# Kernel tuning notes

Hardware: AMD Instinct MI355X
Metric: run time of the kernel (lower is better)

The kernel has to match this reference:

```python
import jax, jax.numpy as jnp
import numpy as np

VOC, TOPIC, EMB, BATCH = 128000, 512, 1024, 1024

def setup_inputs() -> dict:
    key = jax.random.key(0)
    k1, k2, k3 = jax.random.split(key, 3)
    x = jax.random.normal(k1, (TOPIC, BATCH), dtype=jnp.float32)
    beta0 = jax.random.normal(k2, (VOC, EMB), dtype=jnp.float32)
    beta_t = jax.random.normal(k3, (TOPIC, EMB), dtype=jnp.float32) * 0.02  # nn.init.normal_(std=0.02)
    return {"x": x, "beta0": beta0, "beta_t": beta_t, "t": 0}

def reference(x, beta0, beta_t, t):
    # w: [voc, topic] = beta0 [voc, emb] @ beta_t.T [emb, topic]
    # (the t==0 branch and else branch are identical in the source)
    w = jnp.einsum('ve,te->vt', beta0, beta_t)
    w = jax.nn.softmax(w, axis=0)  # softmax over vocab dim (dim=0)
    # out: [voc, batch]
    return jnp.einsum('vt,tb->vb', w, x)
```

## Files before the change

kernel.cpp:

```cpp
#include <hip/hip_runtime.h>

typedef _Float16 f16x8 __attribute__((ext_vector_type(8)));
typedef float    f32x4 __attribute__((ext_vector_type(4)));
typedef unsigned short u16;

#define VOC   128000
#define TOPIC 512
#define EMB   1024
#define BATCH 1024
#define ROWB  128

__device__ __forceinline__ int swz(int row, int kbyte) {
    return row * ROWB + (kbyte ^ ((row & 7) << 4));
}
__device__ __forceinline__ int xcd_swz(int bid, int nwg) {
    return (bid & 7) * (nwg >> 3) + (bid >> 3);
}
union H2U { _Float16 h; u16 u; };

__global__ void cvt_betat_kernel(const float* __restrict__ betat, u16* __restrict__ bt16) {
    const size_t g = (size_t)blockIdx.x * 256 + threadIdx.x;
    const float4* src = reinterpret_cast<const float4*>(betat) + g * 2;
    float4 a = src[0], b = src[1];
    f16x8 h;
    h[0]=(_Float16)a.x; h[1]=(_Float16)a.y; h[2]=(_Float16)a.z; h[3]=(_Float16)a.w;
    h[4]=(_Float16)b.x; h[5]=(_Float16)b.y; h[6]=(_Float16)b.z; h[7]=(_Float16)b.w;
    *(reinterpret_cast<f16x8*>(bt16) + g) = h;
}

__global__ __launch_bounds__(512, 2) void gemm1_kernel(
    const float* __restrict__ beta0, const u16* __restrict__ bt16,
    u16* __restrict__ Eg, size_t TSTR, int RSTR, float* __restrict__ sg)
{
    __shared__ char lds[49152];
    char* ldsA = lds;
    char* ldsB = lds + 16384;

    const int tid  = threadIdx.x;
    const int lane = tid & 63;
    const int wid  = tid >> 6;
    const int wr = wid >> 2, wc = wid & 3;
    const int lr = lane & 15, lk = lane >> 4;
    const int srow8  = lane >> 3;
    const int schunk = ((lane & 7) ^ srow8) * 8;

    const int bid  = xcd_swz(blockIdx.x, gridDim.x);
    const int t0   = (bid & 1) * 256;
    const int tile = bid >> 1;
    const int v0   = tile * 128;

    const int arow = tid >> 2;
    const int asp  = (tid & 3) * 2;

    f32x4 acc[4][4] = {};
    float4 rA[4];

    auto loadA = [&](int kt) {
        const float4* g = reinterpret_cast<const float4*>(
            beta0 + (size_t)(v0 + arow) * EMB + kt * 64 + asp * 8);
        rA[0] = g[0]; rA[1] = g[1]; rA[2] = g[2]; rA[3] = g[3];
    };

    loadA(0);

    for (int kt = 0; kt < EMB / 64; ++kt) {
        __syncthreads();
        const u16* bsrc = bt16 + (size_t)(t0 + wid * 8 + srow8) * EMB + kt * 64 + schunk;
        #pragma unroll
        for (int p = 0; p < 4; ++p) {
            __builtin_amdgcn_global_load_lds(
                (const __attribute__((address_space(1))) unsigned int*)(bsrc + (size_t)p * 64 * EMB),
                (__attribute__((address_space(3))) unsigned int*)(ldsB + (p * 64 + wid * 8) * ROWB),
                16, 0, 0);
        }
        {
            f16x8 h;
            h[0]=(_Float16)rA[0].x; h[1]=(_Float16)rA[0].y; h[2]=(_Float16)rA[0].z; h[3]=(_Float16)rA[0].w;
            h[4]=(_Float16)rA[1].x; h[5]=(_Float16)rA[1].y; h[6]=(_Float16)rA[1].z; h[7]=(_Float16)rA[1].w;
            *reinterpret_cast<f16x8*>(ldsA + swz(arow, asp * 16)) = h;
            f16x8 h2;
            h2[0]=(_Float16)rA[2].x; h2[1]=(_Float16)rA[2].y; h2[2]=(_Float16)rA[2].z; h2[3]=(_Float16)rA[2].w;
            h2[4]=(_Float16)rA[3].x; h2[5]=(_Float16)rA[3].y; h2[6]=(_Float16)rA[3].z; h2[7]=(_Float16)rA[3].w;
            *reinterpret_cast<f16x8*>(ldsA + swz(arow, (asp + 1) * 16)) = h2;
        }
        if (kt + 1 < EMB / 64) loadA(kt + 1);
        __syncthreads();
        #pragma unroll
        for (int ks = 0; ks < 2; ++ks) {
            f16x8 af[4], bf[4];
            #pragma unroll
            for (int m = 0; m < 4; ++m)
                af[m] = *reinterpret_cast<const f16x8*>(ldsA + swz(wr * 64 + m * 16 + lr, ks * 64 + lk * 16));
            #pragma unroll
            for (int n = 0; n < 4; ++n)
                bf[n] = *reinterpret_cast<const f16x8*>(ldsB + swz(wc * 64 + n * 16 + lr, ks * 64 + lk * 16));
            #pragma unroll
            for (int m = 0; m < 4; ++m)
                #pragma unroll
                for (int n = 0; n < 4; ++n)
                    acc[m][n] = __builtin_amdgcn_mfma_f32_16x16x32_f16(
                        af[m], bf[n], acc[m][n], 0, 0, 0);
        }
    }

    __syncthreads();
    u16* ldsE = reinterpret_cast<u16*>(lds);
    float csum = 0.f;
    #pragma unroll
    for (int c = 0; c < 2; ++c) {
        if (wr == c) {
            #pragma unroll
            for (int m = 0; m < 4; ++m)
              #pragma unroll
              for (int n = 0; n < 4; ++n)
                #pragma unroll
                for (int r = 0; r < 4; ++r) {
                    const int row = m * 16 + lk * 4 + r;
                    const int col = wc * 64 + n * 16 + lr;
                    H2U cv; cv.h = (_Float16)__expf(acc[m][n][r]);
                    ldsE[row * 264 + col] = cv.u;
                }
        }
        __syncthreads();
        {
            const int row8 = tid >> 3, seg = tid & 7;
            const int4* srcp = reinterpret_cast<const int4*>(&ldsE[row8 * 264 + seg * 32]);
            u16* dst = Eg + tile * TSTR + (size_t)(c * 64 + row8) * RSTR + t0 + seg * 32;
            int4 v0v = srcp[0], v1v = srcp[1], v2v = srcp[2], v3v = srcp[3];
            int4* dp = reinterpret_cast<int4*>(dst);
            dp[0] = v0v; dp[1] = v1v; dp[2] = v2v; dp[3] = v3v;
        }
        if (tid < 256) {
            float s = 0.f;
            for (int r = 0; r < 64; ++r) { H2U cv; cv.u = ldsE[r * 264 + tid]; s += (float)cv.h; }
            csum += s;
        }
        __syncthreads();
    }
    if (tid < 256) atomicAdd(sg + t0 + tid, csum);
}

__global__ void xst_kernel(const float* __restrict__ x, const float* __restrict__ s,
                           u16* __restrict__ xsT)
{
    __shared__ float tile[32][33];
    const int b0 = blockIdx.x * 32, t0 = blockIdx.y * 32;
    const int tx = threadIdx.x, ty = threadIdx.y;
    tile[ty][tx] = x[(size_t)(t0 + ty) * BATCH + b0 + tx];
    __syncthreads();
    const float sc = 65536.0f / s[t0 + tx];
    H2U cv; cv.h = (_Float16)(tile[tx][ty] * sc);
    xsT[(size_t)(b0 + ty) * TOPIC + t0 + tx] = cv.u;
}

__global__ __launch_bounds__(512, 2) void gemm2a_kernel(
    const u16* __restrict__ Eg, size_t TSTR, int RSTR,
    const u16* __restrict__ xsT, float* __restrict__ out, int c0, int nch)
{
    __shared__ char lds[49152];
    char* ldsA = lds;
    char* ldsB = lds + 16384;

    const int tid  = threadIdx.x;
    const int lane = tid & 63;
    const int wid  = tid >> 6;
    const int wr = wid >> 2, wc = wid & 3;
    const int lr = lane & 15, lk = lane >> 4;
    const int srow8  = lane >> 3;
    const int schunk = ((lane & 7) ^ srow8) * 8;

    const int bid   = xcd_swz(blockIdx.x, gridDim.x);
    const int tile  = bid / nch;
    const int chunk = bid % nch;
    const int b0    = c0 + chunk * 256;
    const int v0    = tile * 128;
    const u16* Et   = Eg + tile * TSTR;

    f32x4 acc[4][4] = {};

    for (int kt = 0; kt < TOPIC / 64; ++kt) {
        const int k0 = kt * 64;
        __syncthreads();
        #pragma unroll
        for (int p = 0; p < 2; ++p) {
            const int rbase = p * 64 + wid * 8;
            __builtin_amdgcn_global_load_lds(
                (const __attribute__((address_space(1))) unsigned int*)
                    (Et + (size_t)(rbase + srow8) * RSTR + k0 + schunk),
                (__attribute__((address_space(3))) unsigned int*)(ldsA + rbase * ROWB),
                16, 0, 0);
        }
        #pragma unroll
        for (int p = 0; p < 4; ++p) {
            const int rbase = p * 64 + wid * 8;
            __builtin_amdgcn_global_load_lds(
                (const __attribute__((address_space(1))) unsigned int*)
                    (xsT + (size_t)(b0 + rbase + srow8) * TOPIC + k0 + schunk),
                (__attribute__((address_space(3))) unsigned int*)(ldsB + rbase * ROWB),
                16, 0, 0);
        }
        __syncthreads();
        #pragma unroll
        for (int ks = 0; ks < 2; ++ks) {
            f16x8 af[4], bf[4];
            #pragma unroll
            for (int m = 0; m < 4; ++m)
                af[m] = *reinterpret_cast<const f16x8*>(ldsA + swz(wr * 64 + m * 16 + lr, ks * 64 + lk * 16));
            #pragma unroll
            for (int n = 0; n < 4; ++n)
                bf[n] = *reinterpret_cast<const f16x8*>(ldsB + swz(wc * 64 + n * 16 + lr, ks * 64 + lk * 16));
            #pragma unroll
            for (int m = 0; m < 4; ++m)
                #pragma unroll
                for (int n = 0; n < 4; ++n)
                    acc[m][n] = __builtin_amdgcn_mfma_f32_16x16x32_f16(
                        af[m], bf[n], acc[m][n], 0, 0, 0);
        }
    }

    #pragma unroll
    for (int m = 0; m < 4; ++m)
      #pragma unroll
      for (int n = 0; n < 4; ++n)
        #pragma unroll
        for (int r = 0; r < 4; ++r) {
            const int row = wr * 64 + m * 16 + lk * 4 + r;
            const int col = wc * 64 + n * 16 + lr;
            out[(size_t)(v0 + row) * BATCH + b0 + col] = acc[m][n][r] * 0x1p-16f;
        }
}

__global__ __launch_bounds__(512, 1) void gemm2b_kernel(
    const u16* __restrict__ EgBase,
    const u16* __restrict__ xsT, float* __restrict__ out)
{
    __shared__ char ldsB[32768];

    const int tid  = threadIdx.x;
    const int lane = tid & 63;
    const int wid  = tid >> 6;
    const int wr = wid >> 2, wc = wid & 3;
    const int lr = lane & 15, lk = lane >> 4;

    const int bid  = xcd_swz(blockIdx.x, gridDim.x);
    const int tile = bid >> 1;
    const int h    = bid & 1;
    const u16* Et  = EgBase + (size_t)tile * 262144;

    f16x8 af[2][16];
    #pragma unroll
    for (int m = 0; m < 2; ++m) {
        const int row = h * 64 + wr * 32 + m * 16 + lr;
        #pragma unroll
        for (int kb = 0; kb < 16; ++kb)
            af[m][kb] = *reinterpret_cast<const f16x8*>(
                Et + (size_t)row * 2048 + kb * 32 + lk * 8);
    }
    asm volatile("s_waitcnt vmcnt(0)" ::: "memory");
    __syncthreads();

    f32x4 acc[2][4] = {};
    for (int kt = 0; kt < 8; ++kt) {
        __syncthreads();
        {
            const int srow = tid >> 1;
            const int sp   = (tid & 1) * 4;
            const u16* g = xsT + (size_t)srow * TOPIC + kt * 64 + sp * 8;
            const int4* gv = reinterpret_cast<const int4*>(g);
            int4 a = gv[0], b = gv[1], cc = gv[2], d = gv[3];
            *reinterpret_cast<int4*>(ldsB + swz(srow, (sp + 0) * 16)) = a;
            *reinterpret_cast<int4*>(ldsB + swz(srow, (sp + 1) * 16)) = b;
            *reinterpret_cast<int4*>(ldsB + swz(srow, (sp + 2) * 16)) = cc;
            *reinterpret_cast<int4*>(ldsB + swz(srow, (sp + 3) * 16)) = d;
        }
        __syncthreads();
        #pragma unroll
        for (int kk = 0; kk < 2; ++kk) {
            f16x8 bf[4];
            #pragma unroll
            for (int n = 0; n < 4; ++n)
                bf[n] = *reinterpret_cast<const f16x8*>(ldsB + swz(wc * 64 + n * 16 + lr, kk * 64 + lk * 16));
            #pragma unroll
            for (int m = 0; m < 2; ++m)
                #pragma unroll
                for (int n = 0; n < 4; ++n)
                    acc[m][n] = __builtin_amdgcn_mfma_f32_16x16x32_f16(
                        af[m][kt * 2 + kk], bf[n], acc[m][n], 0, 0, 0);
        }
    }

    #pragma unroll
    for (int m = 0; m < 2; ++m)
      #pragma unroll
      for (int n = 0; n < 4; ++n)
        #pragma unroll
        for (int r = 0; r < 4; ++r) {
            const int row = h * 64 + wr * 32 + m * 16 + lk * 4 + r;
            const int col = wc * 64 + n * 16 + lr;
            out[((size_t)tile * 128 + row) * BATCH + col] = acc[m][n][r] * 0x1p-16f;
        }
}

extern "C" void kernel_launch(void* const* d_in, const int* in_sizes, int n_in,
                              void* d_out, int out_size, void* d_ws, size_t ws_size,
                              hipStream_t stream)
{
    const float* x     = (const float*)d_in[0];
    const float* beta0 = (const float*)d_in[1];
    const float* betat = (const float*)d_in[2];
    float* out = (float*)d_out;

    const size_t need_min = 4096 + (size_t)BATCH * TOPIC * 2;
    if (ws_size < need_min) return;
    float* s_g  = (float*)d_ws;
    u16*   buf1 = (u16*)((char*)d_ws + 4096);

    const size_t E_OFF = 4u * 1024u * 1024u;
    const bool big = ws_size >= E_OFF + (size_t)VOC * TOPIC * 2;

    hipMemsetAsync(d_ws, 0, 2048, stream);
    cvt_betat_kernel<<<256, 256, 0, stream>>>(betat, buf1);

    if (big) {
        u16* EgW = (u16*)((char*)d_ws + E_OFF);
        gemm1_kernel<<<2000, 512, 0, stream>>>(beta0, buf1, EgW, (size_t)128 * 512, 512, s_g);
        xst_kernel<<<dim3(BATCH / 32, TOPIC / 32), dim3(32, 32), 0, stream>>>(x, s_g, buf1);
        gemm2a_kernel<<<4000, 512, 0, stream>>>(EgW, (size_t)128 * 512, 512, buf1, out, 0, 4);
    } else {
        u16* EgO = (u16*)d_out;
        gemm1_kernel<<<2000, 512, 0, stream>>>(beta0, buf1, EgO, (size_t)262144, 2048, s_g);
        xst_kernel<<<dim3(BATCH / 32, TOPIC / 32), dim3(32, 32), 0, stream>>>(x, s_g, buf1);
        gemm2a_kernel<<<3000, 512, 0, stream>>>(EgO, (size_t)262144, 2048, buf1, out, 256, 3);
        gemm2b_kernel<<<2000, 512, 0, stream>>>(EgO, buf1, out);
    }
}
```

Baseline: 582.0 us.

## Double-buffer LDS tiles in all three GEMM kernels to overlap loads with MFMA

Adds ping-pong LDS buffers in gemm1, gemm2a and gemm2b so the global-to-LDS loads for the next K tile are issued before the MFMA work on the current tile. The __syncthreads pairs are replaced by raw s_barrier plus explicit vmcnt/lgkmcnt waits. gemm2b also moves to register prefetch of x and raises its launch-bounds occupancy hint to 2. The aim is to hide global load latency. In exchange, LDS per block doubles to 96 KB in gemm1 and gemm2a, which may cut occupancy below the requested 2 blocks per CU. The hand-written waits also risk subtle races.

```diff
diff --git a/kernel.cpp b/kernel.cpp
--- a/kernel.cpp
+++ b/kernel.cpp
@@ -17,6 +17,10 @@
     return (bid & 7) * (nwg >> 3) + (bid >> 3);
 }
 union H2U { _Float16 h; u16 u; };
+
+#define SBAR() asm volatile("s_barrier" ::: "memory")
+#define WVM0() asm volatile("s_waitcnt vmcnt(0)" ::: "memory")
+#define WLG0() asm volatile("s_waitcnt lgkmcnt(0)" ::: "memory")
 
 __global__ void cvt_betat_kernel(const float* __restrict__ betat, u16* __restrict__ bt16) {
     const size_t g = (size_t)blockIdx.x * 256 + threadIdx.x;
@@ -32,9 +36,7 @@
     const float* __restrict__ beta0, const u16* __restrict__ bt16,
     u16* __restrict__ Eg, size_t TSTR, int RSTR, float* __restrict__ sg)
 {
-    __shared__ char lds[49152];
-    char* ldsA = lds;
-    char* ldsB = lds + 16384;
+    __shared__ char lds[98304];
 
     const int tid  = threadIdx.x;
     const int lane = tid & 63;
@@ -60,19 +62,27 @@
             beta0 + (size_t)(v0 + arow) * EMB + kt * 64 + asp * 8);
         rA[0] = g[0]; rA[1] = g[1]; rA[2] = g[2]; rA[3] = g[3];
     };
-
-    loadA(0);
-
-    for (int kt = 0; kt < EMB / 64; ++kt) {
-        __syncthreads();
+    auto issueB = [&](int kt, int buf) {
         const u16* bsrc = bt16 + (size_t)(t0 + wid * 8 + srow8) * EMB + kt * 64 + schunk;
-        #pragma unroll
-        for (int p = 0; p < 4; ++p) {
+        char* dstb = lds + 32768 + buf * 32768;
+        #pragma unroll
+        for (int p = 0; p < 4; ++p)
             __builtin_amdgcn_global_load_lds(
                 (const __attribute__((address_space(1))) unsigned int*)(bsrc + (size_t)p * 64 * EMB),
-                (__attribute__((address_space(3))) unsigned int*)(ldsB + (p * 64 + wid * 8) * ROWB),
+                (__attribute__((address_space(3))) unsigned int*)(dstb + (p * 64 + wid * 8) * ROWB),
                 16, 0, 0);
-        }
+    };
+
+    issueB(0, 0);
+    loadA(0);
+
+    for (int kt = 0; kt < EMB / 64; ++kt) {
+        const int cur = kt & 1;
+        char* ldsA = lds + cur * 16384;
+        char* ldsB = lds + 32768 + cur * 32768;
+
+        SBAR();
+        WVM0();
         {
             f16x8 h;
             h[0]=(_Float16)rA[0].x; h[1]=(_Float16)rA[0].y; h[2]=(_Float16)rA[0].z; h[3]=(_Float16)rA[0].w;
@@ -83,8 +93,9 @@
             h2[4]=(_Float16)rA[3].x; h2[5]=(_Float16)rA[3].y; h2[6]=(_Float16)rA[3].z; h2[7]=(_Float16)rA[3].w;
             *reinterpret_cast<f16x8*>(ldsA + swz(arow, (asp + 1) * 16)) = h2;
         }
-        if (kt + 1 < EMB / 64) loadA(kt + 1);
-        __syncthreads();
+        if (kt + 1 < EMB / 64) { issueB(kt + 1, cur ^ 1); loadA(kt + 1); }
+        WLG0();
+        SBAR();
         #pragma unroll
         for (int ks = 0; ks < 2; ++ks) {
             f16x8 af[4], bf[4];
@@ -157,9 +168,7 @@
     const u16* __restrict__ Eg, size_t TSTR, int RSTR,
     const u16* __restrict__ xsT, float* __restrict__ out, int c0, int nch)
 {
-    __shared__ char lds[49152];
-    char* ldsA = lds;
-    char* ldsB = lds + 16384;
+    __shared__ char lds[98304];
 
     const int tid  = threadIdx.x;
     const int lane = tid & 63;
@@ -178,16 +187,17 @@
 
     f32x4 acc[4][4] = {};
 
-    for (int kt = 0; kt < TOPIC / 64; ++kt) {
+    auto issueAB = [&](int kt, int buf) {
         const int k0 = kt * 64;
-        __syncthreads();
+        char* dA = lds + buf * 16384;
+        char* dB = lds + 32768 + buf * 32768;
         #pragma unroll
         for (int p = 0; p < 2; ++p) {
             const int rbase = p * 64 + wid * 8;
             __builtin_amdgcn_global_load_lds(
                 (const __attribute__((address_space(1))) unsigned int*)
                     (Et + (size_t)(rbase + srow8) * RSTR + k0 + schunk),
-                (__attribute__((address_space(3))) unsigned int*)(ldsA + rbase * ROWB),
+                (__attribute__((address_space(3))) unsigned int*)(dA + rbase * ROWB),
                 16, 0, 0);
         }
         #pragma unroll
@@ -196,10 +206,22 @@
             __builtin_amdgcn_global_load_lds(
                 (const __attribute__((address_space(1))) unsigned int*)
                     (xsT + (size_t)(b0 + rbase + srow8) * TOPIC + k0 + schunk),
-                (__attribute__((address_space(3))) unsigned int*)(ldsB + rbase * ROWB),
+                (__attribute__((address_space(3))) unsigned int*)(dB + rbase * ROWB),
                 16, 0, 0);
         }
-        __syncthreads();
+    };
+
+    issueAB(0, 0);
+
+    for (int kt = 0; kt < TOPIC / 64; ++kt) {
+        const int cur = kt & 1;
+        char* ldsA = lds + cur * 16384;
+        char* ldsB = lds + 32768 + cur * 32768;
+
+        SBAR();
+        WVM0();
+        if (kt + 1 < TOPIC / 64) issueAB(kt + 1, cur ^ 1);
+        SBAR();
         #pragma unroll
         for (int ks = 0; ks < 2; ++ks) {
             f16x8 af[4], bf[4];
@@ -230,11 +252,11 @@
         }
 }
 
-__global__ __launch_bounds__(512, 1) void gemm2b_kernel(
+__global__ __launch_bounds__(512, 2) void gemm2b_kernel(
     const u16* __restrict__ EgBase,
     const u16* __restrict__ xsT, float* __restrict__ out)
 {
-    __shared__ char ldsB[32768];
+    __shared__ char lds[65536];
 
     const int tid  = threadIdx.x;
     const int lane = tid & 63;
@@ -256,24 +278,37 @@
             af[m][kb] = *reinterpret_cast<const f16x8*>(
                 Et + (size_t)row * 2048 + kb * 32 + lk * 8);
     }
-    asm volatile("s_waitcnt vmcnt(0)" ::: "memory");
+    WVM0();
     __syncthreads();
+
+    int4 rX[4];
+    auto loadX = [&](int kt) {
+        const int srow = tid >> 1;
+        const int sp   = (tid & 1) * 4;
+        const int4* gv = reinterpret_cast<const int4*>(
+            xsT + (size_t)srow * TOPIC + kt * 64 + sp * 8);
+        rX[0] = gv[0]; rX[1] = gv[1]; rX[2] = gv[2]; rX[3] = gv[3];
+    };
+    loadX(0);
 
     f32x4 acc[2][4] = {};
     for (int kt = 0; kt < 8; ++kt) {
-        __syncthreads();
+        const int cur = kt & 1;
+        char* ldsB = lds + cur * 32768;
+
+        SBAR();
+        WVM0();
         {
             const int srow = tid >> 1;
             const int sp   = (tid & 1) * 4;
-            const u16* g = xsT + (size_t)srow * TOPIC + kt * 64 + sp * 8;
-            const int4* gv = reinterpret_cast<const int4*>(g);
-            int4 a = gv[0], b = gv[1], cc = gv[2], d = gv[3];
-            *reinterpret_cast<int4*>(ldsB + swz(srow, (sp + 0) * 16)) = a;
-            *reinterpret_cast<int4*>(ldsB + swz(srow, (sp + 1) * 16)) = b;
-            *reinterpret_cast<int4*>(ldsB + swz(srow, (sp + 2) * 16)) = cc;
-            *reinterpret_cast<int4*>(ldsB + swz(srow, (sp + 3) * 16)) = d;
-        }
-        __syncthreads();
+            *reinterpret_cast<int4*>(ldsB + swz(srow, (sp + 0) * 16)) = rX[0];
+            *reinterpret_cast<int4*>(ldsB + swz(srow, (sp + 1) * 16)) = rX[1];
+            *reinterpret_cast<int4*>(ldsB + swz(srow, (sp + 2) * 16)) = rX[2];
+            *reinterpret_cast<int4*>(ldsB + swz(srow, (sp + 3) * 16)) = rX[3];
+        }
+        if (kt + 1 < 8) loadX(kt + 1);
+        WLG0();
+        SBAR();
         #pragma unroll
         for (int kk = 0; kk < 2; ++kk) {
             f16x8 bf[4];
```

Result: faster. 515.4 us (-11.4%).
